# Kernel optimization log

Hardware: AMD Instinct MI355X
Metric: run time of the kernel (lower is better)

The kernel has to match this reference:

```python
import jax, jax.numpy as jnp
import numpy as np

N, E, D = 20000, 320000, 128
TD, AD, RH, Z = 16, 16, 256, 64
RIN = 2 * RH // 2 + TD + AD  # 256 + 16 + 16 = 288


def _w(k, shape):
    # torch-style [out, in] weight, scaled by 1/sqrt(fan_in)
    return jax.random.normal(k, shape, jnp.float32) / np.sqrt(shape[-1])


def setup_inputs() -> dict:
    key = jax.random.key(0)
    ks = jax.random.split(key, 32)
    inp = {
        "x": jax.random.normal(ks[0], (N, D), jnp.float32),
        "t": jax.random.normal(ks[1], (N, TD), jnp.float32),
        "a": jax.random.normal(ks[2], (N, AD), jnp.float32),
        "eps": jax.random.normal(ks[3], (N, Z), jnp.float32),
        "edge_index": jax.random.randint(ks[4], (2, E), 0, N, jnp.int64)
        if jax.config.jax_enable_x64 else jax.random.randint(ks[4], (2, E), 0, N, jnp.int32),
        "enc_w1": _w(ks[5], (256, 2 * D)), "enc_b1": jnp.zeros((256,), jnp.float32),
        "enc_w2": _w(ks[6], (256, 256)), "enc_b2": jnp.zeros((256,), jnp.float32),
        "hi_w0": _w(ks[7], (RH, 288)), "hi_b0": jnp.zeros((RH,), jnp.float32),
        "hi_w1": _w(ks[8], (RH, 288)), "hi_b1": jnp.zeros((RH,), jnp.float32),
        "gru_wih0": _w(ks[9], (3 * RH, 288)), "gru_whh0": _w(ks[10], (3 * RH, RH)),
        "gru_bih0": jnp.zeros((3 * RH,), jnp.float32), "gru_bhh0": jnp.zeros((3 * RH,), jnp.float32),
        "gru_wih1": _w(ks[11], (3 * RH, RH)), "gru_whh1": _w(ks[12], (3 * RH, RH)),
        "gru_bih1": jnp.zeros((3 * RH,), jnp.float32), "gru_bhh1": jnp.zeros((3 * RH,), jnp.float32),
        "mu_w": _w(ks[13], (Z, RH)), "mu_b": jnp.zeros((Z,), jnp.float32),
        "lv_w": _w(ks[14], (Z, RH)), "lv_b": jnp.zeros((Z,), jnp.float32),
    }
    return inp


def _gru_cell(xin, h, wih, whh, bih, bhh):
    gi = xin @ wih.T + bih          # [N, 3H]
    gh = h @ whh.T + bhh            # [N, 3H]
    i_r, i_z, i_n = jnp.split(gi, 3, axis=-1)
    h_r, h_z, h_n = jnp.split(gh, 3, axis=-1)
    r = jax.nn.sigmoid(i_r + h_r)
    zg = jax.nn.sigmoid(i_z + h_z)
    n = jnp.tanh(i_n + r * h_n)
    return (1.0 - zg) * n + zg * h


def reference(x, t, a, eps, edge_index,
              enc_w1, enc_b1, enc_w2, enc_b2,
              hi_w0, hi_b0, hi_w1, hi_b1,
              gru_wih0, gru_whh0, gru_bih0, gru_bhh0,
              gru_wih1, gru_whh1, gru_bih1, gru_bhh1,
              mu_w, mu_b, lv_w, lv_b):
    n_nodes = x.shape[0]
    src, dst = edge_index[0], edge_index[1]
    # EdgeConv: nn(cat([x_i, x_j - x_i])) with max aggregation at target i
    x_i = x[dst]                                   # [E, D]
    x_j = x[src]                                   # [E, D]
    m = jnp.concatenate([x_i, x_j - x_i], axis=-1)  # [E, 2D]
    m = jax.nn.relu(m @ enc_w1.T + enc_b1)
    m = jax.nn.relu(m @ enc_w2.T + enc_b2)          # [E, 256]
    agg = jax.ops.segment_max(m, dst, num_segments=n_nodes)
    agg = jnp.where(jnp.isneginf(agg), 0.0, agg)    # nodes w/o edges -> 0
    feat = jnp.concatenate([agg, t, a], axis=-1)    # [N, 288]
    # initial hidden per GRU layer from rnn_hi MLPs (h is None branch)
    h0 = jnp.tanh(feat @ hi_w0.T + hi_b0)           # [N, 256]
    h1 = jnp.tanh(feat @ hi_w1.T + hi_b1)
    # single GRU step, 2 layers (nodes act as batch)
    new_h0 = _gru_cell(feat, h0, gru_wih0, gru_whh0, gru_bih0, gru_bhh0)
    new_h1 = _gru_cell(new_h0, h1, gru_wih1, gru_whh1, gru_bih1, gru_bhh1)
    h = jnp.stack([new_h0, new_h1], axis=0)         # [2, N, 256]
    data = new_h1
    mu = data @ mu_w.T + mu_b                        # [N, 64]
    log_var = data @ lv_w.T + lv_b
    std = jnp.exp(0.5 * log_var)
    z = mu + eps * std
    return h, mu, log_var, z
```

## Files before the change

kernel.cpp:

```cpp
#include <hip/hip_runtime.h>
#include <math.h>

#define N_NODES 20000
#define N_EDGES 320000

typedef __attribute__((ext_vector_type(8))) short bf16x8;
typedef __attribute__((ext_vector_type(4))) float f32x4;
typedef unsigned short ushort_t;
typedef unsigned int uint_t;

__device__ __forceinline__ float bf2f(uint_t u) {
    uint_t i = u << 16; float f; __builtin_memcpy(&f, &i, 4); return f;
}
__device__ __forceinline__ ushort_t f2bf(float f) {
    uint_t i; __builtin_memcpy(&i, &f, 4);
    uint_t r = i + 0x7fffu + ((i >> 16) & 1u);
    return (ushort_t)(r >> 16);
}

__global__ void pack_all(const float* __restrict__ w1, const float* __restrict__ b1,
                         const float* __restrict__ w2,
                         const float* __restrict__ hiw0, const float* __restrict__ hiw1,
                         const float* __restrict__ wih0, const float* __restrict__ whh0,
                         const float* __restrict__ wih1, const float* __restrict__ whh1,
                         const float* __restrict__ muw, const float* __restrict__ lvw,
                         const float* __restrict__ mub, const float* __restrict__ lvb,
                         ushort_t* __restrict__ pk, float* __restrict__ bpq)
{
    const int w = blockIdx.y;
    const int i = blockIdx.x * 256 + threadIdx.x;
    if (w == 9) {
        if (i < 256)      bpq[i] = b1[i];
        else if (i < 512) bpq[i] = 0.0f;
        else if (i < 576) bpq[i] = mub[i - 512];
        else if (i < 640) bpq[i] = lvb[i - 576];
        return;
    }
    const int Ks[9]  = {128, 256, 288, 288, 288, 256, 256, 256, 256};
    const int NOs[9] = {512, 256, 256, 256, 768, 768, 768, 768, 128};
    const int DST[9] = {0, 65536, 131072, 204800, 278528, 499712, 696320, 892928, 1089536};
    const float* srcs[9] = {w1, w2, hiw0, hiw1, wih0, whh0, wih1, whh1, muw};
    const int K = Ks[w], NO = NOs[w];
    if (i >= (K * NO) >> 3) return;
    const int lane = i & 63, rest = i >> 6, NOT = NO >> 4;
    const int ot = rest % NOT, k0 = rest / NOT;
    const int row = ot * 16 + (lane & 15);
    const int kb = k0 * 32 + (lane >> 4) * 8;
    ushort_t o[8];
    if (w == 0) {
#pragma unroll
        for (int j = 0; j < 8; ++j) {
            int k = kb + j;
            float v = (row < 256) ? (w1[row * 256 + k] - w1[row * 256 + 128 + k])
                                  : w1[(row - 256) * 256 + 128 + k];
            o[j] = f2bf(v);
        }
    } else if (w == 8) {
#pragma unroll
        for (int j = 0; j < 8; ++j) {
            float v = (row < 64) ? muw[row * 256 + kb + j] : lvw[(row - 64) * 256 + kb + j];
            o[j] = f2bf(v);
        }
    } else {
        const float* s = srcs[w];
#pragma unroll
        for (int j = 0; j < 8; ++j) o[j] = f2bf(s[(size_t)row * K + kb + j]);
    }
    ushort_t* d = pk + DST[w] + (size_t)i * 8;
    ((uint_t*)d)[0] = (uint_t)o[0] | ((uint_t)o[1] << 16);
    ((uint_t*)d)[1] = (uint_t)o[2] | ((uint_t)o[3] << 16);
    ((uint_t*)d)[2] = (uint_t)o[4] | ((uint_t)o[5] << 16);
    ((uint_t*)d)[3] = (uint_t)o[6] | ((uint_t)o[7] << 16);
}

__global__ void xcvt(const float* __restrict__ x, ushort_t* __restrict__ xbf)
{
    int base = (blockIdx.x * 256 + threadIdx.x) * 4;
    if (base >= N_NODES * 128) return;
    float4 v = *(const float4*)&x[base];
    uint2 u;
    u.x = (uint_t)f2bf(v.x) | ((uint_t)f2bf(v.y) << 16);
    u.y = (uint_t)f2bf(v.z) | ((uint_t)f2bf(v.w) << 16);
    *(uint2*)&xbf[base] = u;
}

template <int BN, int OMODE>
__global__ __launch_bounds__(256) void mgemm(
    const ushort_t* __restrict__ Abf, int lda, int M, int K,
    const ushort_t* __restrict__ Wp, int NOtot, const float* __restrict__ bias,
    float* __restrict__ Cf, ushort_t* __restrict__ Cbf, int ldc)
{
    __shared__ char smem[40960];
    const int tid = threadIdx.x;
    const int l = tid & 63, wid = tid >> 6;
    const int m0 = blockIdx.x * 64;
    const int n0 = blockIdx.y * BN;
    const int RS = (K * 2 + 127) & ~127;
    const int CHR = K >> 3;
    for (int c = tid; c < 64 * CHR; c += 256) {
        int row = c / CHR, cb = c - row * CHR;
        int gr = m0 + row; if (gr >= M) gr = M - 1;
        bf16x8 v = *(const bf16x8*)&Abf[(size_t)gr * lda + cb * 8];
        *(bf16x8*)&smem[row * RS + ((cb * 16) ^ ((row & 7) << 4))] = v;
    }
    __syncthreads();

    constexpr int NT = BN / 16;
    f32x4 acc[NT];
#pragma unroll
    for (int j = 0; j < NT; ++j) acc[j] = (f32x4){0.f, 0.f, 0.f, 0.f};
    const int rw = wid * 16 + (l & 15);
    const int hi = l >> 4;
    const int swz = (rw & 7) << 4;
    const int KB = K >> 5;
    const int otb = n0 >> 4;
    for (int k0 = 0; k0 < KB; ++k0) {
        bf16x8 a = *(const bf16x8*)&smem[rw * RS + ((k0 * 64 + hi * 16) ^ swz)];
        const ushort_t* wb = Wp + ((size_t)(k0 * NOtot + otb) * 64 + l) * 8;
#pragma unroll
        for (int j = 0; j < NT; ++j) {
            bf16x8 b = *(const bf16x8*)&wb[(size_t)j * 512];
            acc[j] = __builtin_amdgcn_mfma_f32_16x16x32_bf16(a, b, acc[j], 0, 0, 0);
        }
    }
    const int c0 = l & 15;
    const int r0 = m0 + wid * 16 + hi * 4;
#pragma unroll
    for (int j = 0; j < NT; ++j) {
        float bj = bias[n0 + j * 16 + c0];
#pragma unroll
        for (int r = 0; r < 4; ++r) {
            int gr = r0 + r;
            if (gr >= M) continue;
            float v = acc[j][r] + bj;
            if (OMODE == 2) v = tanhf(v);
            if (OMODE == 3) {
                int col = n0 + j * 16 + c0;
                size_t o = (size_t)gr * 64 + (col & 63) + ((col >= 64) ? (size_t)M * 64 : 0);
                Cf[o] = v;
            } else {
                size_t o = (size_t)gr * ldc + n0 + j * 16 + c0;
                if (OMODE == 0) Cf[o] = v;
                else if (OMODE == 1) Cbf[o] = f2bf(v);
                else { Cf[o] = v; Cbf[o] = f2bf(v); }
            }
        }
    }
}

__global__ __launch_bounds__(256) void edge_mfma(
    const ushort_t* __restrict__ PQbf,
    const int* __restrict__ ei,
    const ushort_t* __restrict__ W2p,
    const float* __restrict__ b2,
    float* __restrict__ agg)
{
    __shared__ char h1s[16384];
    __shared__ int s_dst[32], s_src[32];
    const int tid = threadIdx.x;
    const int e0 = blockIdx.x * 32;
    if (tid < 32) {
        int d = ei[N_EDGES + e0 + tid];
        s_dst[tid] = min(max(d, 0), N_NODES - 1);
    } else if (tid < 64) {
        int s = ei[e0 + tid - 32];
        s_src[tid - 32] = min(max(s, 0), N_NODES - 1);
    }
    __syncthreads();

    const int wv = tid >> 6;
    const int ln = tid & 63;
#pragma unroll 4
    for (int eb = wv; eb < 32; eb += 4) {
        int dst = s_dst[eb], src = s_src[eb];
        uint2 pu = *(const uint2*)&PQbf[(size_t)dst * 512 + ln * 4];
        uint2 qu = *(const uint2*)&PQbf[(size_t)src * 512 + 256 + ln * 4];
        float v0 = fmaxf(bf2f(pu.x & 0xffffu) + bf2f(qu.x & 0xffffu), 0.f);
        float v1 = fmaxf(bf2f(pu.x >> 16)     + bf2f(qu.x >> 16),     0.f);
        float v2 = fmaxf(bf2f(pu.y & 0xffffu) + bf2f(qu.y & 0xffffu), 0.f);
        float v3 = fmaxf(bf2f(pu.y >> 16)     + bf2f(qu.y >> 16),     0.f);
        uint2 hv;
        hv.x = (uint_t)f2bf(v0) | ((uint_t)f2bf(v1) << 16);
        hv.y = (uint_t)f2bf(v2) | ((uint_t)f2bf(v3) << 16);
        *(uint2*)&h1s[eb * 512 + ((ln * 8) ^ ((eb & 7) << 4))] = hv;
    }
    __syncthreads();

    const int l = tid & 63, wid = tid >> 6;
    const int rw = (wid & 1) * 16 + (l & 15);
    const int hi = l >> 4;
    const int swz = (rw & 7) << 4;
    const int otb = (wid >> 1) * 8;
    f32x4 acc[8];
#pragma unroll
    for (int j = 0; j < 8; ++j) acc[j] = (f32x4){0.f, 0.f, 0.f, 0.f};
    for (int k0 = 0; k0 < 8; ++k0) {
        bf16x8 a = *(const bf16x8*)&h1s[rw * 512 + ((k0 * 64 + hi * 16) ^ swz)];
        const ushort_t* wb = W2p + ((size_t)(k0 * 16 + otb) * 64 + l) * 8;
#pragma unroll
        for (int j = 0; j < 8; ++j) {
            bf16x8 b = *(const bf16x8*)&wb[(size_t)j * 512];
            acc[j] = __builtin_amdgcn_mfma_f32_16x16x32_bf16(a, b, acc[j], 0, 0, 0);
        }
    }
    const int c0 = l & 15;
    const int edg = (wid & 1) * 16 + hi * 4;
#pragma unroll
    for (int j = 0; j < 8; ++j) {
        int col = (otb + j) * 16 + c0;
        float bj = b2[col];
#pragma unroll
        for (int r = 0; r < 4; ++r) {
            float v = acc[j][r] + bj;
            if (v > 0.f) {
                int node = s_dst[edg + r];
                atomicMax((int*)&agg[(size_t)node * 256 + col], __float_as_int(v));
            }
        }
    }
}

__global__ void build_feat(const float* __restrict__ agg, const float* __restrict__ t,
                           const float* __restrict__ a, ushort_t* __restrict__ featbf)
{
    int idx = blockIdx.x * 256 + threadIdx.x;
    if (idx >= N_NODES * 288) return;
    int n = idx / 288, c = idx - n * 288;
    float v;
    if (c < 256)      v = agg[(size_t)n * 256 + c];
    else if (c < 272) v = t[n * 16 + (c - 256)];
    else              v = a[n * 16 + (c - 272)];
    featbf[idx] = f2bf(v);
}

__global__ __launch_bounds__(256) void gru_fused(
    const ushort_t* __restrict__ A1, int K1,
    const ushort_t* __restrict__ A2,
    const ushort_t* __restrict__ Wp1,
    const ushort_t* __restrict__ Wp2,
    const float* __restrict__ bih, const float* __restrict__ bhh,
    const float* __restrict__ hf,
    float* __restrict__ houtf,
    ushort_t* __restrict__ houtb)
{
    __shared__ char smem[40960];
    const int tid = threadIdx.x;
    const int l = tid & 63, wid = tid >> 6;
    const int m0 = blockIdx.x * 64;
    const int n0 = blockIdx.y * 64;
    const int rw = wid * 16 + (l & 15);
    const int hi = l >> 4;
    const int swz = (rw & 7) << 4;
    const int otb = n0 >> 4;

    f32x4 aR[4], aZ[4], aN[4], bR[4], bZ[4], bN[4];
#pragma unroll
    for (int j = 0; j < 4; ++j) {
        aR[j] = (f32x4){0.f,0.f,0.f,0.f}; aZ[j] = aR[j]; aN[j] = aR[j];
        bR[j] = aR[j]; bZ[j] = aR[j]; bN[j] = aR[j];
    }

    {
        const int RS = (K1 * 2 + 127) & ~127;
        const int CHR = K1 >> 3;
        for (int c = tid; c < 64 * CHR; c += 256) {
            int row = c / CHR, cb = c - row * CHR;
            int gr = m0 + row; if (gr >= N_NODES) gr = N_NODES - 1;
            bf16x8 v = *(const bf16x8*)&A1[(size_t)gr * K1 + cb * 8];
            *(bf16x8*)&smem[row * RS + ((cb * 16) ^ ((row & 7) << 4))] = v;
        }
        __syncthreads();
        const int KB = K1 >> 5;
        for (int k0 = 0; k0 < KB; ++k0) {
            bf16x8 a = *(const bf16x8*)&smem[rw * RS + ((k0 * 64 + hi * 16) ^ swz)];
            const ushort_t* wb = Wp1 + ((size_t)(k0 * 48) * 64 + l) * 8;
#pragma unroll
            for (int j = 0; j < 4; ++j) {
                bf16x8 b0 = *(const bf16x8*)&wb[(size_t)(otb + j) * 512];
                aR[j] = __builtin_amdgcn_mfma_f32_16x16x32_bf16(a, b0, aR[j], 0, 0, 0);
                bf16x8 b1 = *(const bf16x8*)&wb[(size_t)(16 + otb + j) * 512];
                aZ[j] = __builtin_amdgcn_mfma_f32_16x16x32_bf16(a, b1, aZ[j], 0, 0, 0);
                bf16x8 b2 = *(const bf16x8*)&wb[(size_t)(32 + otb + j) * 512];
                aN[j] = __builtin_amdgcn_mfma_f32_16x16x32_bf16(a, b2, aN[j], 0, 0, 0);
            }
        }
    }
    __syncthreads();
    {
        for (int c = tid; c < 64 * 32; c += 256) {
            int row = c >> 5, cb = c & 31;
            int gr = m0 + row; if (gr >= N_NODES) gr = N_NODES - 1;
            bf16x8 v = *(const bf16x8*)&A2[(size_t)gr * 256 + cb * 8];
            *(bf16x8*)&smem[row * 512 + ((cb * 16) ^ ((row & 7) << 4))] = v;
        }
        __syncthreads();
        for (int k0 = 0; k0 < 8; ++k0) {
            bf16x8 a = *(const bf16x8*)&smem[rw * 512 + ((k0 * 64 + hi * 16) ^ swz)];
            const ushort_t* wb = Wp2 + ((size_t)(k0 * 48) * 64 + l) * 8;
#pragma unroll
            for (int j = 0; j < 4; ++j) {
                bf16x8 b0 = *(const bf16x8*)&wb[(size_t)(otb + j) * 512];
                bR[j] = __builtin_amdgcn_mfma_f32_16x16x32_bf16(a, b0, bR[j], 0, 0, 0);
                bf16x8 b1 = *(const bf16x8*)&wb[(size_t)(16 + otb + j) * 512];
                bZ[j] = __builtin_amdgcn_mfma_f32_16x16x32_bf16(a, b1, bZ[j], 0, 0, 0);
                bf16x8 b2 = *(const bf16x8*)&wb[(size_t)(32 + otb + j) * 512];
                bN[j] = __builtin_amdgcn_mfma_f32_16x16x32_bf16(a, b2, bN[j], 0, 0, 0);
            }
        }
    }
    const int c0 = l & 15;
    const int r0 = m0 + wid * 16 + hi * 4;
#pragma unroll
    for (int j = 0; j < 4; ++j) {
        int col = n0 + j * 16 + c0;
        float br_ = bih[col], bz_ = bih[256 + col], bn_ = bih[512 + col];
        float cr_ = bhh[col], cz_ = bhh[256 + col], cn_ = bhh[512 + col];
#pragma unroll
        for (int r = 0; r < 4; ++r) {
            int gr = r0 + r;
            if (gr >= N_NODES) continue;
            float ir = aR[j][r] + br_, iz = aZ[j][r] + bz_, in_ = aN[j][r] + bn_;
            float hr = bR[j][r] + cr_, hz = bZ[j][r] + cz_, hn = bN[j][r] + cn_;
            float h = hf[(size_t)gr * 256 + col];
            float rg = 1.f / (1.f + expf(-(ir + hr)));
            float zg = 1.f / (1.f + expf(-(iz + hz)));
            float ng = tanhf(in_ + rg * hn);
            float v = (1.f - zg) * ng + zg * h;
            houtf[(size_t)gr * 256 + col] = v;
            houtb[(size_t)gr * 256 + col] = f2bf(v);
        }
    }
}

__global__ void z_kernel(const float* __restrict__ mu, const float* __restrict__ lv,
                         const float* __restrict__ eps, float* __restrict__ z)
{
    int idx = blockIdx.x * 256 + threadIdx.x;
    if (idx >= N_NODES * 64) return;
    z[idx] = mu[idx] + eps[idx] * expf(0.5f * lv[idx]);
}

extern "C" void kernel_launch(void* const* d_in, const int* in_sizes, int n_in,
                              void* d_out, int out_size, void* d_ws, size_t ws_size,
                              hipStream_t stream)
{
    const float* x      = (const float*)d_in[0];
    const float* t      = (const float*)d_in[1];
    const float* a      = (const float*)d_in[2];
    const float* eps    = (const float*)d_in[3];
    const int*   ei     = (const int*)d_in[4];
    const float* enc_w1 = (const float*)d_in[5];
    const float* enc_b1 = (const float*)d_in[6];
    const float* enc_w2 = (const float*)d_in[7];
    const float* enc_b2 = (const float*)d_in[8];
    const float* hi_w0  = (const float*)d_in[9];
    const float* hi_b0  = (const float*)d_in[10];
    const float* hi_w1  = (const float*)d_in[11];
    const float* hi_b1  = (const float*)d_in[12];
    const float* wih0   = (const float*)d_in[13];
    const float* whh0   = (const float*)d_in[14];
    const float* bih0   = (const float*)d_in[15];
    const float* bhh0   = (const float*)d_in[16];
    const float* wih1   = (const float*)d_in[17];
    const float* whh1   = (const float*)d_in[18];
    const float* bih1   = (const float*)d_in[19];
    const float* bhh1   = (const float*)d_in[20];
    const float* mu_w   = (const float*)d_in[21];
    const float* mu_b   = (const float*)d_in[22];
    const float* lv_w   = (const float*)d_in[23];
    const float* lv_b   = (const float*)d_in[24];

    char* W = (char*)d_ws;
    ushort_t* pk     = (ushort_t*)(W + 0);
    float*    bpq    = (float*)(W + 2244608);
    ushort_t* xbf    = (ushort_t*)(W + 2247680);
    float*    agg    = (float*)(W + 7368704);
    float*    h0f    = (float*)(W + 7368704);
    ushort_t* pqbf   = (ushort_t*)(W + 27848704);
    float*    h1f    = (float*)(W + 27848704);
    ushort_t* featbf = (ushort_t*)(W + 48328704);
    ushort_t* h0bf   = (ushort_t*)(W + 59848704);
    ushort_t* h1bf   = (ushort_t*)(W + 70088704);
    ushort_t* nh0bf  = (ushort_t*)(W + 80328704);
    ushort_t* nh1bf  = (ushort_t*)(W + 90568704);

    float* out_h0 = (float*)d_out;
    float* out_h1 = out_h0 + (size_t)N_NODES * 256;
    float* out_mu = out_h1 + (size_t)N_NODES * 256;
    float* out_lv = out_mu + (size_t)N_NODES * 64;
    float* out_z  = out_lv + (size_t)N_NODES * 64;

    dim3 blk(256);

    pack_all<<<dim3(108, 10), blk, 0, stream>>>(enc_w1, enc_b1, enc_w2, hi_w0, hi_w1,
                                                wih0, whh0, wih1, whh1, mu_w, lv_w,
                                                mu_b, lv_b, pk, bpq);
    xcvt<<<2500, blk, 0, stream>>>(x, xbf);
    hipMemsetAsync(agg, 0, (size_t)N_NODES * 256 * sizeof(float), stream);

    mgemm<128, 1><<<dim3(313, 4), blk, 0, stream>>>(xbf, 128, N_NODES, 128,
                                                    pk + 0, 32, bpq, nullptr, pqbf, 512);
    edge_mfma<<<10000, blk, 0, stream>>>(pqbf, ei, pk + 65536, enc_b2, agg);

    build_feat<<<22500, blk, 0, stream>>>(agg, t, a, featbf);

    mgemm<128, 2><<<dim3(313, 2), blk, 0, stream>>>(featbf, 288, N_NODES, 288,
                                                    pk + 131072, 16, hi_b0, h0f, h0bf, 256);
    mgemm<128, 2><<<dim3(313, 2), blk, 0, stream>>>(featbf, 288, N_NODES, 288,
                                                    pk + 204800, 16, hi_b1, h1f, h1bf, 256);
    gru_fused<<<dim3(313, 4), blk, 0, stream>>>(featbf, 288, h0bf,
                                                pk + 278528, pk + 499712,
                                                bih0, bhh0, h0f, out_h0, nh0bf);
    gru_fused<<<dim3(313, 4), blk, 0, stream>>>(nh0bf, 256, h1bf,
                                                pk + 696320, pk + 892928,
                                                bih1, bhh1, h1f, out_h1, nh1bf);
    mgemm<64, 3><<<dim3(313, 2), blk, 0, stream>>>(nh1bf, 256, N_NODES, 256,
                                                   pk + 1089536, 8, bpq + 512,
                                                   out_mu, nullptr, 64);
    z_kernel<<<5000, blk, 0, stream>>>(out_mu, out_lv, eps, out_z);
}
```

Measured before the change: 701.1 us.

## Fuse reparameterization into mu/logvar GEMM and pre-check atomicMax

The mu/log_var GEMM now computes both 64-wide heads in one block (128 output columns) and applies z = mu + eps*exp(0.5*lv) in its epilogue, removing the separate z kernel and the reload of mu/lv. The edge kernel also reads the current aggregate value and skips the atomicMax when the new value is not larger, which is meant to cut atomic traffic on heavily contended destinations. The plain read can be stale, but that stays correct because the atomic is still issued whenever the value might be larger. The eps pointer is passed through the bf16 output argument with a cast, which is awkward but functional.

```diff
diff --git a/kernel.cpp b/kernel.cpp
--- a/kernel.cpp
+++ b/kernel.cpp
@@ -125,6 +125,26 @@
     }
     const int c0 = l & 15;
     const int r0 = m0 + wid * 16 + hi * 4;
+    if (OMODE == 4) {
+        const float* epsp = (const float*)Cbf;
+#pragma unroll
+        for (int j = 0; j < 4; ++j) {
+            int c = j * 16 + c0;
+            float bmu = bias[c], blv = bias[64 + c];
+#pragma unroll
+            for (int r = 0; r < 4; ++r) {
+                int gr = r0 + r;
+                if (gr >= M) continue;
+                float mu = acc[j][r] + bmu;
+                float lv = acc[j + 4][r] + blv;
+                float e  = epsp[(size_t)gr * 64 + c];
+                Cf[(size_t)gr * 64 + c] = mu;
+                Cf[(size_t)M * 64 + (size_t)gr * 64 + c] = lv;
+                Cf[(size_t)2 * M * 64 + (size_t)gr * 64 + c] = mu + e * expf(0.5f * lv);
+            }
+        }
+        return;
+    }
 #pragma unroll
     for (int j = 0; j < NT; ++j) {
         float bj = bias[n0 + j * 16 + c0];
@@ -134,16 +154,10 @@
             if (gr >= M) continue;
             float v = acc[j][r] + bj;
             if (OMODE == 2) v = tanhf(v);
-            if (OMODE == 3) {
-                int col = n0 + j * 16 + c0;
-                size_t o = (size_t)gr * 64 + (col & 63) + ((col >= 64) ? (size_t)M * 64 : 0);
-                Cf[o] = v;
-            } else {
-                size_t o = (size_t)gr * ldc + n0 + j * 16 + c0;
-                if (OMODE == 0) Cf[o] = v;
-                else if (OMODE == 1) Cbf[o] = f2bf(v);
-                else { Cf[o] = v; Cbf[o] = f2bf(v); }
-            }
+            size_t o = (size_t)gr * ldc + n0 + j * 16 + c0;
+            if (OMODE == 0) Cf[o] = v;
+            else if (OMODE == 1) Cbf[o] = f2bf(v);
+            else { Cf[o] = v; Cbf[o] = f2bf(v); }
         }
     }
 }
@@ -214,7 +228,9 @@
             float v = acc[j][r] + bj;
             if (v > 0.f) {
                 int node = s_dst[edg + r];
-                atomicMax((int*)&agg[(size_t)node * 256 + col], __float_as_int(v));
+                int* addr = (int*)&agg[(size_t)node * 256 + col];
+                int iv = __float_as_int(v);
+                if (iv > *addr) atomicMax(addr, iv);
             }
         }
     }
@@ -330,14 +346,6 @@
             houtb[(size_t)gr * 256 + col] = f2bf(v);
         }
     }
-}
-
-__global__ void z_kernel(const float* __restrict__ mu, const float* __restrict__ lv,
-                         const float* __restrict__ eps, float* __restrict__ z)
-{
-    int idx = blockIdx.x * 256 + threadIdx.x;
-    if (idx >= N_NODES * 64) return;
-    z[idx] = mu[idx] + eps[idx] * expf(0.5f * lv[idx]);
 }
 
 extern "C" void kernel_launch(void* const* d_in, const int* in_sizes, int n_in,
@@ -387,8 +395,6 @@
     float* out_h0 = (float*)d_out;
     float* out_h1 = out_h0 + (size_t)N_NODES * 256;
     float* out_mu = out_h1 + (size_t)N_NODES * 256;
-    float* out_lv = out_mu + (size_t)N_NODES * 64;
-    float* out_z  = out_lv + (size_t)N_NODES * 64;
 
     dim3 blk(256);
 
@@ -414,8 +420,7 @@
     gru_fused<<<dim3(313, 4), blk, 0, stream>>>(nh0bf, 256, h1bf,
                                                 pk + 696320, pk + 892928,
                                                 bih1, bhh1, h1f, out_h1, nh1bf);
-    mgemm<64, 3><<<dim3(313, 2), blk, 0, stream>>>(nh1bf, 256, N_NODES, 256,
-                                                   pk + 1089536, 8, bpq + 512,
-                                                   out_mu, nullptr, 64);
-    z_kernel<<<5000, blk, 0, stream>>>(out_mu, out_lv, eps, out_z);
-}
+    mgemm<128, 4><<<dim3(313, 1), blk, 0, stream>>>(nh1bf, 256, N_NODES, 256,
+                                                    pk + 1089536, 8, bpq + 512,
+                                                    out_mu, (ushort_t*)eps, 64);
+}
```

Measured after the change: 803.4 us. +14.6%, slower.
